# Kernel tuning notes

Measured on AMD Instinct MI355X. Metric: run time of the kernel, lower is better.

The kernel has to match this reference:

```python
import jax, jax.numpy as jnp
import numpy as np

T = 8192  # context/question length (input_shape[2])
D = 128   # feature dim (input_shape[3])


def setup_inputs() -> dict:
    key = jax.random.key(0)
    k1, k2 = jax.random.split(key)
    x = jax.random.normal(k1, (2, 1, T, D), dtype=jnp.float32)
    kernel = jax.random.normal(k2, (3 * D,), dtype=jnp.float32)
    return {"x": x, "kernel": kernel}


def reference(x, kernel):
    context = x[0, 0]   # (T, D)
    question = x[1, 0]  # (T, D)
    w_c, w_q, w_m = kernel[:D], kernel[D:2 * D], kernel[2 * D:]

    # Additive similarity: S[i,j] = c_i.w_c + q_j.w_q + (c_i*q_j).w_m
    # Avoids materializing the (T, T, 3D) tiled/concatenated tensor.
    S = (context @ w_c)[:, None] + (question @ w_q)[None, :] \
        + (context * w_m) @ question.T  # (T, T)

    A = jax.nn.softmax(S, axis=-1)  # row-wise softmax, as tf.nn.softmax on 2D

    # C2Q attention: U_A[i] = sum_j A[i,j] * q_j
    U_A = A @ question  # (T, D)

    # Q2C attention: b = row-max of A, h = sum_i b_i * c_i, tiled over rows
    b = jnp.max(A, axis=1)          # (T,)
    h = b @ context                 # (D,)
    H_A = jnp.broadcast_to(h, (T, D))

    # megamerge: [c, U_A, c*U_A, c*H_A]
    G = jnp.concatenate([context, U_A, context * U_A, context * H_A], axis=-1)
    return G  # (T, 4D)
```

## Files before the change

kernel.cpp:

```cpp
#include <hip/hip_runtime.h>
#include <hip/hip_bf16.h>

#define T 8192
#define D 128
#define NSPLIT 8
#define JLEN (T / NSPLIT)
#define BN 64
#define NITER (JLEN / BN)
#define BM 128
#define LOG2E 1.44269504088896f

typedef _Float16 half2_t __attribute__((ext_vector_type(2)));
typedef _Float16 half4_t __attribute__((ext_vector_type(4)));
typedef _Float16 half8_t __attribute__((ext_vector_type(8)));
typedef __fp16 fp16x2_t __attribute__((ext_vector_type(2)));
typedef float floatx4 __attribute__((ext_vector_type(4)));
typedef float floatx16 __attribute__((ext_vector_type(16)));

__global__ void prep_kernel(const float* __restrict__ x, const float* __restrict__ kern,
                            _Float16* __restrict__ q16, _Float16* __restrict__ qT16,
                            _Float16* __restrict__ cm16, float* __restrict__ qq2,
                            float* __restrict__ h) {
    const float* context  = x;
    const float* question = x + (size_t)T * D;
    const float* wq = kern + D;
    const float* wm = kern + 2 * D;
    __shared__ __align__(16) _Float16 tile[32][136];
    int j0 = blockIdx.x * 32;
    int t = threadIdx.x;
    if (blockIdx.x == 0 && t < 128) h[t] = 0.f;
    int c4 = t & 31;
    int rsub = t >> 5;
    float4 wqv = ((const float4*)wq)[c4];
    float4 wmv = ((const float4*)wm)[c4];
    for (int p = 0; p < 4; ++p) {
        int row = p * 8 + rsub;
        float4 q = ((const float4*)(question + (size_t)(j0 + row) * D))[c4];
        float4 c = ((const float4*)(context  + (size_t)(j0 + row) * D))[c4];
        half4_t qh;
        qh[0] = (_Float16)q.x; qh[1] = (_Float16)q.y; qh[2] = (_Float16)q.z; qh[3] = (_Float16)q.w;
        *(half4_t*)(q16 + (size_t)(j0 + row) * D + c4 * 4) = qh;
        *(half4_t*)&tile[row][c4 * 4] = qh;
        half4_t ch;
        ch[0] = (_Float16)(c.x * wmv.x * LOG2E); ch[1] = (_Float16)(c.y * wmv.y * LOG2E);
        ch[2] = (_Float16)(c.z * wmv.z * LOG2E); ch[3] = (_Float16)(c.w * wmv.w * LOG2E);
        *(half4_t*)(cm16 + (size_t)(j0 + row) * D + c4 * 4) = ch;
        float s = q.x * wqv.x + q.y * wqv.y + q.z * wqv.z + q.w * wqv.w;
        for (int dx = 1; dx <= 16; dx <<= 1) s += __shfl_xor(s, dx);
        if (c4 == 0) qq2[j0 + row] = s * LOG2E;
    }
    __syncthreads();
    for (int p = 0; p < 2; ++p) {
        int chunk = t + p * 256;
        int d = chunk >> 2, jo = (chunk & 3) * 8;
        half8_t v;
        for (int s2 = 0; s2 < 8; ++s2) v[s2] = tile[jo + s2][d];
        *(half8_t*)(qT16 + (size_t)d * T + j0 + jo) = v;
    }
}

__global__ __launch_bounds__(256, 2)
void flash_kernel(const _Float16* __restrict__ q16, const _Float16* __restrict__ qT16,
                  const _Float16* __restrict__ cm16, const float* __restrict__ qq2,
                  unsigned char* __restrict__ Opart, float* __restrict__ mpart,
                  float* __restrict__ lpart) {
    __shared__ __align__(16) _Float16 Kt[2][64][136];
    __shared__ __align__(16) _Float16 Vt[2][128][64];
    __shared__ __align__(16) float qqs[JLEN];

    const int bx = blockIdx.x;
    const int rb = bx >> 3;
    const int sp = bx & 7;
    const int tid = threadIdx.x;
    const int wave = tid >> 6;
    const int lane = tid & 63;
    const int l31 = lane & 31;
    const int h = lane >> 5;
    const int rbase = rb * BM + wave * 32;
    const int q = rbase + l31;
    const int sig = (l31 & 19) | ((l31 & 4) << 1) | ((l31 & 8) >> 1);

    ((float4*)qqs)[tid] = ((const float4*)(qq2 + (size_t)sp * JLEN))[tid];

    half8_t qfrag[8];
#pragma unroll
    for (int ks = 0; ks < 8; ++ks)
        qfrag[ks] = *(const half8_t*)(cm16 + (size_t)q * D + ks * 16 + h * 8);

    floatx16 acc[4];
#pragma unroll
    for (int nt = 0; nt < 4; ++nt)
#pragma unroll
        for (int r = 0; r < 16; ++r) acc[nt][r] = 0.f;
    float m_run = -INFINITY, l_run = 0.f;

    const int j0 = sp * JLEN;
    half8_t kreg[4], vreg[4];
#pragma unroll
    for (int k = 0; k < 4; ++k) {
        int idx = tid + k * 256;
        kreg[k] = *(const half8_t*)(q16 + (size_t)(j0 + (idx >> 4)) * D + (idx & 15) * 8);
        vreg[k] = *(const half8_t*)(qT16 + (size_t)(idx >> 3) * T + j0 + (idx & 7) * 8);
    }
#pragma unroll
    for (int k = 0; k < 4; ++k) {
        int idx = tid + k * 256;
        *(half8_t*)&Kt[0][idx >> 4][(idx & 15) * 8] = kreg[k];
        int dr = idx >> 3, c8 = idx & 7;
        *(half8_t*)&Vt[0][dr][((c8 + (dr & 7)) & 7) * 8] = vreg[k];
    }
#pragma unroll
    for (int k = 0; k < 4; ++k) {
        int idx = tid + k * 256;
        kreg[k] = *(const half8_t*)(q16 + (size_t)(j0 + BN + (idx >> 4)) * D + (idx & 15) * 8);
        vreg[k] = *(const half8_t*)(qT16 + (size_t)(idx >> 3) * T + j0 + BN + (idx & 7) * 8);
    }
    __syncthreads();

    floatx16 Sp[2];
#pragma unroll
    for (int jt = 0; jt < 2; ++jt) {
        const float* qb = &qqs[jt * 32];
        float4 b0 = *(const float4*)(qb + 8 * h);
        float4 b1 = *(const float4*)(qb + 4 + 8 * h);
        float4 b2 = *(const float4*)(qb + 16 + 8 * h);
        float4 b3 = *(const float4*)(qb + 20 + 8 * h);
        Sp[jt][0]  = b0.x; Sp[jt][1]  = b0.y; Sp[jt][2]  = b0.z; Sp[jt][3]  = b0.w;
        Sp[jt][4]  = b1.x; Sp[jt][5]  = b1.y; Sp[jt][6]  = b1.z; Sp[jt][7]  = b1.w;
        Sp[jt][8]  = b2.x; Sp[jt][9]  = b2.y; Sp[jt][10] = b2.z; Sp[jt][11] = b2.w;
        Sp[jt][12] = b3.x; Sp[jt][13] = b3.y; Sp[jt][14] = b3.z; Sp[jt][15] = b3.w;
#pragma unroll
        for (int ks = 0; ks < 8; ++ks) {
            half8_t a = *(const half8_t*)&Kt[0][jt * 32 + sig][ks * 16 + h * 8];
            Sp[jt] = __builtin_amdgcn_mfma_f32_32x32x16_f16(a, qfrag[ks], Sp[jt], 0, 0, 0);
        }
    }

    for (int it = 0; it < NITER; ++it) {
        const int cur = it & 1;
        if (it + 1 < NITER) {
#pragma unroll
            for (int k = 0; k < 4; ++k) {
                int idx = tid + k * 256;
                *(half8_t*)&Kt[cur ^ 1][idx >> 4][(idx & 15) * 8] = kreg[k];
            }
        }
        __syncthreads();
        if (it + 1 < NITER) {
#pragma unroll
            for (int k = 0; k < 4; ++k) {
                int idx = tid + k * 256;
                int dr = idx >> 3, c8 = idx & 7;
                *(half8_t*)&Vt[cur ^ 1][dr][((c8 + (dr & 7)) & 7) * 8] = vreg[k];
            }
        }
        if (it + 2 < NITER) {
            int jn = j0 + (it + 2) * BN;
#pragma unroll
            for (int k = 0; k < 4; ++k) {
                int idx = tid + k * 256;
                kreg[k] = *(const half8_t*)(q16 + (size_t)(jn + (idx >> 4)) * D + (idx & 15) * 8);
                vreg[k] = *(const half8_t*)(qT16 + (size_t)(idx >> 3) * T + jn + (idx & 7) * 8);
            }
        }

        floatx16 Sn[2];
        if (it + 1 < NITER) {
#pragma unroll
            for (int jt = 0; jt < 2; ++jt) {
                const float* qb = &qqs[(it + 1) * 64 + jt * 32];
                float4 b0 = *(const float4*)(qb + 8 * h);
                float4 b1 = *(const float4*)(qb + 4 + 8 * h);
                float4 b2 = *(const float4*)(qb + 16 + 8 * h);
                float4 b3 = *(const float4*)(qb + 20 + 8 * h);
                Sn[jt][0]  = b0.x; Sn[jt][1]  = b0.y; Sn[jt][2]  = b0.z; Sn[jt][3]  = b0.w;
                Sn[jt][4]  = b1.x; Sn[jt][5]  = b1.y; Sn[jt][6]  = b1.z; Sn[jt][7]  = b1.w;
                Sn[jt][8]  = b2.x; Sn[jt][9]  = b2.y; Sn[jt][10] = b2.z; Sn[jt][11] = b2.w;
                Sn[jt][12] = b3.x; Sn[jt][13] = b3.y; Sn[jt][14] = b3.z; Sn[jt][15] = b3.w;
                __builtin_amdgcn_s_setprio(1);
#pragma unroll
                for (int ks = 0; ks < 8; ++ks) {
                    half8_t a = *(const half8_t*)&Kt[cur ^ 1][jt * 32 + sig][ks * 16 + h * 8];
                    Sn[jt] = __builtin_amdgcn_mfma_f32_32x32x16_f16(a, qfrag[ks], Sn[jt], 0, 0, 0);
                }
                __builtin_amdgcn_s_setprio(0);
            }
        }

        float t8[8];
#pragma unroll
        for (int r = 0; r < 8; ++r)
            t8[r] = fmaxf(fmaxf(Sp[0][r], Sp[0][r + 8]), fmaxf(Sp[1][r], Sp[1][r + 8]));
        float mx = fmaxf(fmaxf(fmaxf(t8[0], t8[4]), fmaxf(t8[1], t8[5])),
                         fmaxf(fmaxf(t8[2], t8[6]), fmaxf(t8[3], t8[7])));
        mx = fmaxf(mx, __shfl_xor(mx, 32));
        if (__any(mx > m_run)) {
            float mnew = fmaxf(m_run, mx);
            float alpha = __builtin_amdgcn_exp2f(m_run - mnew);
#pragma unroll
            for (int nt = 0; nt < 4; ++nt)
#pragma unroll
                for (int r = 0; r < 16; ++r) acc[nt][r] *= alpha;
            l_run *= alpha;
            m_run = mnew;
        }
        int pk_[2][2][4];
        float psa[4] = {0.f, 0.f, 0.f, 0.f};
#pragma unroll
        for (int jt = 0; jt < 2; ++jt)
#pragma unroll
            for (int kb = 0; kb < 2; ++kb)
#pragma unroll
                for (int r = 0; r < 4; ++r) {
                    float p0 = __builtin_amdgcn_exp2f(Sp[jt][kb * 8 + 2 * r]     - m_run);
                    float p1 = __builtin_amdgcn_exp2f(Sp[jt][kb * 8 + 2 * r + 1] - m_run);
                    psa[r] += p0 + p1;
                    fp16x2_t pk = __builtin_amdgcn_cvt_pkrtz(p0, p1);
                    pk_[jt][kb][r] = __builtin_bit_cast(int, pk);
                }
        float ps = (psa[0] + psa[1]) + (psa[2] + psa[3]);
        ps += __shfl_xor(ps, 32);
        l_run += ps;

        __builtin_amdgcn_s_setprio(1);
#pragma unroll
        for (int jt = 0; jt < 2; ++jt)
#pragma unroll
            for (int kb = 0; kb < 2; ++kb) {
                int4 w;
                w.x = pk_[jt][kb][0]; w.y = pk_[jt][kb][1];
                w.z = pk_[jt][kb][2]; w.w = pk_[jt][kb][3];
                half8_t pb = __builtin_bit_cast(half8_t, w);
                const int pg = ((jt * 4 + kb * 2 + h) + (l31 & 7)) & 7;
#pragma unroll
                for (int nt = 0; nt < 4; ++nt) {
                    half8_t va = *(const half8_t*)&Vt[cur][nt * 32 + l31][pg * 8];
                    acc[nt] = __builtin_amdgcn_mfma_f32_32x32x16_f16(va, pb, acc[nt], 0, 0, 0);
                }
            }
        __builtin_amdgcn_s_setprio(0);

        if (it + 1 < NITER) { Sp[0] = Sn[0]; Sp[1] = Sn[1]; }
    }

    if (h == 0) {
        mpart[(size_t)sp * T + q] = m_run;
        lpart[(size_t)sp * T + q] = l_run;
    }
    float rinv = 1.0f / l_run;
#pragma unroll
    for (int nt = 0; nt < 4; ++nt)
#pragma unroll
        for (int rg = 0; rg < 4; ++rg) {
            float v0 = acc[nt][rg * 4 + 0] * rinv;
            float v1 = acc[nt][rg * 4 + 1] * rinv;
            float v2 = acc[nt][rg * 4 + 2] * rinv;
            float v3 = acc[nt][rg * 4 + 3] * rinv;
            unsigned u = (unsigned)__builtin_amdgcn_cvt_pk_fp8_f32(v0, v1, 0, false);
            u = (unsigned)__builtin_amdgcn_cvt_pk_fp8_f32(v2, v3, u, true);
            *(unsigned*)(Opart + ((size_t)sp * T + q) * D + nt * 32 + rg * 8 + 4 * h) = u;
        }
}

__global__ void tail_kernel(const unsigned char* __restrict__ Opart, const float* __restrict__ mpart,
                            const float* __restrict__ lpart, const float* __restrict__ x,
                            float* __restrict__ U_A, float* __restrict__ h) {
    __shared__ float linv_s[128];
    int t = threadIdx.x;
    if (blockIdx.x >= 512) {
        int b = blockIdx.x - 512;
        if (t < 128) {
            int i = b * 128 + t;
            float mp[NSPLIT];
            float mstar = -INFINITY;
            for (int sp2 = 0; sp2 < NSPLIT; ++sp2) {
                mp[sp2] = mpart[(size_t)sp2 * T + i];
                mstar = fmaxf(mstar, mp[sp2]);
            }
            float L = 0.f;
            for (int sp2 = 0; sp2 < NSPLIT; ++sp2)
                L += __builtin_amdgcn_exp2f(mp[sp2] - mstar) * lpart[(size_t)sp2 * T + i];
            linv_s[t] = 1.0f / L;
        }
        __syncthreads();
        int d = t & 127, g = t >> 7;
        int r0 = g * 64;
        float s = 0.f;
        for (int r = 0; r < 64; ++r)
            s += x[(size_t)(b * 128 + r0 + r) * D + d] * linv_s[r0 + r];
        atomicAdd(&h[d], s);
        return;
    }
    int i = blockIdx.x * 16 + (t >> 4);
    int c = t & 15;
    float mp[NSPLIT];
    float mstar = -INFINITY;
    for (int sp = 0; sp < NSPLIT; ++sp) {
        mp[sp] = mpart[(size_t)sp * T + i];
        mstar = fmaxf(mstar, mp[sp]);
    }
    float L = 0.f;
    float u[8];
    for (int k = 0; k < 8; ++k) u[k] = 0.f;
    int d0 = c * 8;
    for (int sp = 0; sp < NSPLIT; ++sp) {
        float w = __builtin_amdgcn_exp2f(mp[sp] - mstar) * lpart[(size_t)sp * T + i];
        L += w;
        uint2 ow = *(const uint2*)(Opart + ((size_t)sp * T + i) * D + d0);
        u[0] += __builtin_amdgcn_cvt_f32_fp8(ow.x, 0) * w;
        u[1] += __builtin_amdgcn_cvt_f32_fp8(ow.x, 1) * w;
        u[2] += __builtin_amdgcn_cvt_f32_fp8(ow.x, 2) * w;
        u[3] += __builtin_amdgcn_cvt_f32_fp8(ow.x, 3) * w;
        u[4] += __builtin_amdgcn_cvt_f32_fp8(ow.y, 0) * w;
        u[5] += __builtin_amdgcn_cvt_f32_fp8(ow.y, 1) * w;
        u[6] += __builtin_amdgcn_cvt_f32_fp8(ow.y, 2) * w;
        u[7] += __builtin_amdgcn_cvt_f32_fp8(ow.y, 3) * w;
    }
    float invL = 1.0f / L;
    float4 s0 = make_float4(u[0] * invL, u[1] * invL, u[2] * invL, u[3] * invL);
    float4 s1 = make_float4(u[4] * invL, u[5] * invL, u[6] * invL, u[7] * invL);
    *(float4*)(U_A + (size_t)i * D + d0) = s0;
    *(float4*)(U_A + (size_t)i * D + d0 + 4) = s1;
}

__global__ void assemble_kernel(const float* __restrict__ x, const float* __restrict__ U_A,
                                const float* __restrict__ h, float* __restrict__ out) {
    const float* context = x;
    int gid = blockIdx.x * 256 + threadIdx.x;
    int base = gid * 4;
    int i = base >> 9;
    int c = base & 511;
    int seg = c >> 7, d = c & 127;
    float4 r;
    if (seg == 0) {
        r = *(const float4*)(context + (size_t)i * D + d);
    } else if (seg == 1) {
        r = *(const float4*)(U_A + (size_t)i * D + d);
    } else if (seg == 2) {
        float4 a = *(const float4*)(context + (size_t)i * D + d);
        float4 b = *(const float4*)(U_A + (size_t)i * D + d);
        r = make_float4(a.x * b.x, a.y * b.y, a.z * b.z, a.w * b.w);
    } else {
        float4 a = *(const float4*)(context + (size_t)i * D + d);
        float4 b = *(const float4*)(h + d);
        r = make_float4(a.x * b.x, a.y * b.y, a.z * b.z, a.w * b.w);
    }
    *(float4*)(out + base) = r;
}

extern "C" void kernel_launch(void* const* d_in, const int* in_sizes, int n_in,
                              void* d_out, int out_size, void* d_ws, size_t ws_size,
                              hipStream_t stream) {
    const float* x = (const float*)d_in[0];
    const float* kern = (const float*)d_in[1];
    float* out = (float*)d_out;

    char* w = (char*)d_ws;
    size_t off = 0;
    _Float16* q16  = (_Float16*)(w + off); off += (size_t)T * D * 2;
    _Float16* qT16 = (_Float16*)(w + off); off += (size_t)T * D * 2;
    _Float16* cm16 = (_Float16*)(w + off); off += (size_t)T * D * 2;
    float* qq2   = (float*)(w + off); off += (size_t)T * 4;
    float* mpart = (float*)(w + off); off += (size_t)NSPLIT * T * 4;
    float* lpart = (float*)(w + off); off += (size_t)NSPLIT * T * 4;
    float* U_A   = (float*)(w + off); off += (size_t)T * D * 4;
    float* h     = (float*)(w + off); off += (size_t)D * 4;

    unsigned char* Opart = (unsigned char*)d_out;

    prep_kernel<<<256, 256, 0, stream>>>(x, kern, q16, qT16, cm16, qq2, h);
    flash_kernel<<<512, 256, 0, stream>>>(q16, qT16, cm16, qq2, Opart, mpart, lpart);
    tail_kernel<<<576, 256, 0, stream>>>(Opart, mpart, lpart, x, U_A, h);
    assemble_kernel<<<4096, 256, 0, stream>>>(x, U_A, h, out);
}
```

Measured before the change: 150.4 us.

## Double split count, halve key tile, raise occupancy, drop S prefetch pipeline

Splits the key dimension into 16 chunks instead of 8 and shrinks the key tile from 64 to 32 rows. This doubles the grid and allows four blocks per CU through smaller LDS buffers and a tighter launch bound. The explicit software pipeline that computed the next tile's scores ahead of time is removed: each iteration now computes its own S tile, with a barrier at the end. The intent is to hide latency with more resident waves instead of in-thread prefetch. The cost is more partial results for the tail merge, more barriers per key, and register pressure from the 4-block bound.

After: 184.7 us. +22.8%, slower.

```diff
diff --git a/kernel.cpp b/kernel.cpp
--- a/kernel.cpp
+++ b/kernel.cpp
@@ -3,9 +3,9 @@
 
 #define T 8192
 #define D 128
-#define NSPLIT 8
+#define NSPLIT 16
 #define JLEN (T / NSPLIT)
-#define BN 64
+#define BN 32
 #define NITER (JLEN / BN)
 #define BM 128
 #define LOG2E 1.44269504088896f
@@ -59,18 +59,18 @@
     }
 }
 
-__global__ __launch_bounds__(256, 2)
+__global__ __launch_bounds__(256, 4)
 void flash_kernel(const _Float16* __restrict__ q16, const _Float16* __restrict__ qT16,
                   const _Float16* __restrict__ cm16, const float* __restrict__ qq2,
                   unsigned char* __restrict__ Opart, float* __restrict__ mpart,
                   float* __restrict__ lpart) {
-    __shared__ __align__(16) _Float16 Kt[2][64][136];
-    __shared__ __align__(16) _Float16 Vt[2][128][64];
+    __shared__ __align__(16) _Float16 Kt[2][32][136];
+    __shared__ __align__(16) _Float16 Vt[2][128][32];
     __shared__ __align__(16) float qqs[JLEN];
 
     const int bx = blockIdx.x;
-    const int rb = bx >> 3;
-    const int sp = bx & 7;
+    const int rb = bx >> 4;
+    const int sp = bx & 15;
     const int tid = threadIdx.x;
     const int wave = tid >> 6;
     const int lane = tid & 63;
@@ -80,7 +80,7 @@
     const int q = rbase + l31;
     const int sig = (l31 & 19) | ((l31 & 4) << 1) | ((l31 & 8) >> 1);
 
-    ((float4*)qqs)[tid] = ((const float4*)(qq2 + (size_t)sp * JLEN))[tid];
+    if (tid < 128) ((float4*)qqs)[tid] = ((const float4*)(qq2 + (size_t)sp * JLEN))[tid];
 
     half8_t qfrag[8];
 #pragma unroll
@@ -95,104 +95,74 @@
     float m_run = -INFINITY, l_run = 0.f;
 
     const int j0 = sp * JLEN;
-    half8_t kreg[4], vreg[4];
-#pragma unroll
-    for (int k = 0; k < 4; ++k) {
+    half8_t kreg[2], vreg[2];
+#pragma unroll
+    for (int k = 0; k < 2; ++k) {
         int idx = tid + k * 256;
         kreg[k] = *(const half8_t*)(q16 + (size_t)(j0 + (idx >> 4)) * D + (idx & 15) * 8);
-        vreg[k] = *(const half8_t*)(qT16 + (size_t)(idx >> 3) * T + j0 + (idx & 7) * 8);
-    }
-#pragma unroll
-    for (int k = 0; k < 4; ++k) {
+        vreg[k] = *(const half8_t*)(qT16 + (size_t)(idx >> 2) * T + j0 + (idx & 3) * 8);
+    }
+#pragma unroll
+    for (int k = 0; k < 2; ++k) {
         int idx = tid + k * 256;
         *(half8_t*)&Kt[0][idx >> 4][(idx & 15) * 8] = kreg[k];
-        int dr = idx >> 3, c8 = idx & 7;
-        *(half8_t*)&Vt[0][dr][((c8 + (dr & 7)) & 7) * 8] = vreg[k];
-    }
-#pragma unroll
-    for (int k = 0; k < 4; ++k) {
+        int dr = idx >> 2, c4g = idx & 3;
+        *(half8_t*)&Vt[0][dr][((c4g + (dr & 3)) & 3) * 8] = vreg[k];
+    }
+#pragma unroll
+    for (int k = 0; k < 2; ++k) {
         int idx = tid + k * 256;
         kreg[k] = *(const half8_t*)(q16 + (size_t)(j0 + BN + (idx >> 4)) * D + (idx & 15) * 8);
-        vreg[k] = *(const half8_t*)(qT16 + (size_t)(idx >> 3) * T + j0 + BN + (idx & 7) * 8);
+        vreg[k] = *(const half8_t*)(qT16 + (size_t)(idx >> 2) * T + j0 + BN + (idx & 3) * 8);
     }
     __syncthreads();
-
-    floatx16 Sp[2];
-#pragma unroll
-    for (int jt = 0; jt < 2; ++jt) {
-        const float* qb = &qqs[jt * 32];
-        float4 b0 = *(const float4*)(qb + 8 * h);
-        float4 b1 = *(const float4*)(qb + 4 + 8 * h);
-        float4 b2 = *(const float4*)(qb + 16 + 8 * h);
-        float4 b3 = *(const float4*)(qb + 20 + 8 * h);
-        Sp[jt][0]  = b0.x; Sp[jt][1]  = b0.y; Sp[jt][2]  = b0.z; Sp[jt][3]  = b0.w;
-        Sp[jt][4]  = b1.x; Sp[jt][5]  = b1.y; Sp[jt][6]  = b1.z; Sp[jt][7]  = b1.w;
-        Sp[jt][8]  = b2.x; Sp[jt][9]  = b2.y; Sp[jt][10] = b2.z; Sp[jt][11] = b2.w;
-        Sp[jt][12] = b3.x; Sp[jt][13] = b3.y; Sp[jt][14] = b3.z; Sp[jt][15] = b3.w;
-#pragma unroll
-        for (int ks = 0; ks < 8; ++ks) {
-            half8_t a = *(const half8_t*)&Kt[0][jt * 32 + sig][ks * 16 + h * 8];
-            Sp[jt] = __builtin_amdgcn_mfma_f32_32x32x16_f16(a, qfrag[ks], Sp[jt], 0, 0, 0);
-        }
-    }
 
     for (int it = 0; it < NITER; ++it) {
         const int cur = it & 1;
         if (it + 1 < NITER) {
 #pragma unroll
-            for (int k = 0; k < 4; ++k) {
+            for (int k = 0; k < 2; ++k) {
                 int idx = tid + k * 256;
                 *(half8_t*)&Kt[cur ^ 1][idx >> 4][(idx & 15) * 8] = kreg[k];
-            }
-        }
-        __syncthreads();
-        if (it + 1 < NITER) {
-#pragma unroll
-            for (int k = 0; k < 4; ++k) {
-                int idx = tid + k * 256;
-                int dr = idx >> 3, c8 = idx & 7;
-                *(half8_t*)&Vt[cur ^ 1][dr][((c8 + (dr & 7)) & 7) * 8] = vreg[k];
+                int dr = idx >> 2, c4g = idx & 3;
+                *(half8_t*)&Vt[cur ^ 1][dr][((c4g + (dr & 3)) & 3) * 8] = vreg[k];
             }
         }
         if (it + 2 < NITER) {
             int jn = j0 + (it + 2) * BN;
 #pragma unroll
-            for (int k = 0; k < 4; ++k) {
+            for (int k = 0; k < 2; ++k) {
                 int idx = tid + k * 256;
                 kreg[k] = *(const half8_t*)(q16 + (size_t)(jn + (idx >> 4)) * D + (idx & 15) * 8);
-                vreg[k] = *(const half8_t*)(qT16 + (size_t)(idx >> 3) * T + jn + (idx & 7) * 8);
-            }
-        }
-
-        floatx16 Sn[2];
-        if (it + 1 < NITER) {
-#pragma unroll
-            for (int jt = 0; jt < 2; ++jt) {
-                const float* qb = &qqs[(it + 1) * 64 + jt * 32];
-                float4 b0 = *(const float4*)(qb + 8 * h);
-                float4 b1 = *(const float4*)(qb + 4 + 8 * h);
-                float4 b2 = *(const float4*)(qb + 16 + 8 * h);
-                float4 b3 = *(const float4*)(qb + 20 + 8 * h);
-                Sn[jt][0]  = b0.x; Sn[jt][1]  = b0.y; Sn[jt][2]  = b0.z; Sn[jt][3]  = b0.w;
-                Sn[jt][4]  = b1.x; Sn[jt][5]  = b1.y; Sn[jt][6]  = b1.z; Sn[jt][7]  = b1.w;
-                Sn[jt][8]  = b2.x; Sn[jt][9]  = b2.y; Sn[jt][10] = b2.z; Sn[jt][11] = b2.w;
-                Sn[jt][12] = b3.x; Sn[jt][13] = b3.y; Sn[jt][14] = b3.z; Sn[jt][15] = b3.w;
-                __builtin_amdgcn_s_setprio(1);
-#pragma unroll
-                for (int ks = 0; ks < 8; ++ks) {
-                    half8_t a = *(const half8_t*)&Kt[cur ^ 1][jt * 32 + sig][ks * 16 + h * 8];
-                    Sn[jt] = __builtin_amdgcn_mfma_f32_32x32x16_f16(a, qfrag[ks], Sn[jt], 0, 0, 0);
-                }
-                __builtin_amdgcn_s_setprio(0);
-            }
-        }
-
-        float t8[8];
-#pragma unroll
-        for (int r = 0; r < 8; ++r)
-            t8[r] = fmaxf(fmaxf(Sp[0][r], Sp[0][r + 8]), fmaxf(Sp[1][r], Sp[1][r + 8]));
-        float mx = fmaxf(fmaxf(fmaxf(t8[0], t8[4]), fmaxf(t8[1], t8[5])),
-                         fmaxf(fmaxf(t8[2], t8[6]), fmaxf(t8[3], t8[7])));
+                vreg[k] = *(const half8_t*)(qT16 + (size_t)(idx >> 2) * T + jn + (idx & 3) * 8);
+            }
+        }
+
+        floatx16 St;
+        {
+            const float* qb = &qqs[it * 32];
+            float4 b0 = *(const float4*)(qb + 8 * h);
+            float4 b1 = *(const float4*)(qb + 4 + 8 * h);
+            float4 b2 = *(const float4*)(qb + 16 + 8 * h);
+            float4 b3 = *(const float4*)(qb + 20 + 8 * h);
+            St[0]  = b0.x; St[1]  = b0.y; St[2]  = b0.z; St[3]  = b0.w;
+            St[4]  = b1.x; St[5]  = b1.y; St[6]  = b1.z; St[7]  = b1.w;
+            St[8]  = b2.x; St[9]  = b2.y; St[10] = b2.z; St[11] = b2.w;
+            St[12] = b3.x; St[13] = b3.y; St[14] = b3.z; St[15] = b3.w;
+            __builtin_amdgcn_s_setprio(1);
+#pragma unroll
+            for (int ks = 0; ks < 8; ++ks) {
+                half8_t a = *(const half8_t*)&Kt[cur][sig][ks * 16 + h * 8];
+                St = __builtin_amdgcn_mfma_f32_32x32x16_f16(a, qfrag[ks], St, 0, 0, 0);
+            }
+            __builtin_amdgcn_s_setprio(0);
+        }
+
+        float t4[4];
+#pragma unroll
+        for (int r = 0; r < 4; ++r)
+            t4[r] = fmaxf(fmaxf(St[r], St[r + 4]), fmaxf(St[r + 8], St[r + 12]));
+        float mx = fmaxf(fmaxf(t4[0], t4[1]), fmaxf(t4[2], t4[3]));
         mx = fmaxf(mx, __shfl_xor(mx, 32));
         if (__any(mx > m_run)) {
             float mnew = fmaxf(m_run, mx);
@@ -204,43 +174,38 @@
             l_run *= alpha;
             m_run = mnew;
         }
-        int pk_[2][2][4];
+        int pk_[2][4];
         float psa[4] = {0.f, 0.f, 0.f, 0.f};
 #pragma unroll
-        for (int jt = 0; jt < 2; ++jt)
-#pragma unroll
-            for (int kb = 0; kb < 2; ++kb)
-#pragma unroll
-                for (int r = 0; r < 4; ++r) {
-                    float p0 = __builtin_amdgcn_exp2f(Sp[jt][kb * 8 + 2 * r]     - m_run);
-                    float p1 = __builtin_amdgcn_exp2f(Sp[jt][kb * 8 + 2 * r + 1] - m_run);
-                    psa[r] += p0 + p1;
-                    fp16x2_t pk = __builtin_amdgcn_cvt_pkrtz(p0, p1);
-                    pk_[jt][kb][r] = __builtin_bit_cast(int, pk);
-                }
+        for (int kb = 0; kb < 2; ++kb)
+#pragma unroll
+            for (int r = 0; r < 4; ++r) {
+                float p0 = __builtin_amdgcn_exp2f(St[kb * 8 + 2 * r]     - m_run);
+                float p1 = __builtin_amdgcn_exp2f(St[kb * 8 + 2 * r + 1] - m_run);
+                psa[r] += p0 + p1;
+                fp16x2_t pk = __builtin_amdgcn_cvt_pkrtz(p0, p1);
+                pk_[kb][r] = __builtin_bit_cast(int, pk);
+            }
         float ps = (psa[0] + psa[1]) + (psa[2] + psa[3]);
         ps += __shfl_xor(ps, 32);
         l_run += ps;
 
         __builtin_amdgcn_s_setprio(1);
 #pragma unroll
-        for (int jt = 0; jt < 2; ++jt)
-#pragma unroll
-            for (int kb = 0; kb < 2; ++kb) {
-                int4 w;
-                w.x = pk_[jt][kb][0]; w.y = pk_[jt][kb][1];
-                w.z = pk_[jt][kb][2]; w.w = pk_[jt][kb][3];
-                half8_t pb = __builtin_bit_cast(half8_t, w);
-                const int pg = ((jt * 4 + kb * 2 + h) + (l31 & 7)) & 7;
-#pragma unroll
-                for (int nt = 0; nt < 4; ++nt) {
-                    half8_t va = *(const half8_t*)&Vt[cur][nt * 32 + l31][pg * 8];
-                    acc[nt] = __builtin_amdgcn_mfma_f32_32x32x16_f16(va, pb, acc[nt], 0, 0, 0);
-                }
-            }
+        for (int kb = 0; kb < 2; ++kb) {
+            int4 w;
+            w.x = pk_[kb][0]; w.y = pk_[kb][1];
+            w.z = pk_[kb][2]; w.w = pk_[kb][3];
+            half8_t pb = __builtin_bit_cast(half8_t, w);
+            const int pg = ((kb * 2 + h) + (l31 & 3)) & 3;
+#pragma unroll
+            for (int nt = 0; nt < 4; ++nt) {
+                half8_t va = *(const half8_t*)&Vt[cur][nt * 32 + l31][pg * 8];
+                acc[nt] = __builtin_amdgcn_mfma_f32_32x32x16_f16(va, pb, acc[nt], 0, 0, 0);
+            }
+        }
         __builtin_amdgcn_s_setprio(0);
-
-        if (it + 1 < NITER) { Sp[0] = Sn[0]; Sp[1] = Sn[1]; }
+        __syncthreads();
     }
 
     if (h == 0) {
@@ -369,7 +334,7 @@
     unsigned char* Opart = (unsigned char*)d_out;
 
     prep_kernel<<<256, 256, 0, stream>>>(x, kern, q16, qT16, cm16, qq2, h);
-    flash_kernel<<<512, 256, 0, stream>>>(q16, qT16, cm16, qq2, Opart, mpart, lpart);
+    flash_kernel<<<1024, 256, 0, stream>>>(q16, qT16, cm16, qq2, Opart, mpart, lpart);
     tail_kernel<<<576, 256, 0, stream>>>(Opart, mpart, lpart, x, U_A, h);
     assemble_kernel<<<4096, 256, 0, stream>>>(x, U_A, h, out);
 }
```
